# Kernel tuning notes

Measured on AMD Instinct MI355X. Metric: run time of the kernel, lower is better.

The kernel has to match this reference:

```python
import jax, jax.numpy as jnp
import numpy as np

B, S, V, F, H = 256, 512, 50000, 64, 256


def setup_inputs() -> dict:
    key = jax.random.key(0)
    ks = jax.random.split(key, 12)
    s_in = 1.0 / np.sqrt(F)
    s_hid = 1.0 / np.sqrt(H)
    return {
        "batch": jax.random.randint(ks[0], (B, S), 0, V),
        "features": jax.random.normal(ks[1], (V, F), jnp.float32),
        "W_ih0": jax.random.normal(ks[2], (H, F), jnp.float32) * s_in,
        "W_hh0": jax.random.normal(ks[3], (H, H), jnp.float32) * s_hid,
        "b_ih0": jax.random.normal(ks[4], (H,), jnp.float32) * s_hid,
        "b_hh0": jax.random.normal(ks[5], (H,), jnp.float32) * s_hid,
        "W_ih1": jax.random.normal(ks[6], (H, H), jnp.float32) * s_hid,
        "W_hh1": jax.random.normal(ks[7], (H, H), jnp.float32) * s_hid,
        "b_ih1": jax.random.normal(ks[8], (H,), jnp.float32) * s_hid,
        "b_hh1": jax.random.normal(ks[9], (H,), jnp.float32) * s_hid,
        "W_out": jax.random.normal(ks[10], (V, H), jnp.float32) * s_hid,
        "b_out": jax.random.normal(ks[11], (V,), jnp.float32) * s_hid,
    }


def _rnn_layer(x, W_ih, W_hh, b_ih, b_hh):
    # x: [B, S, Din] -> [B, S, H]; torch tanh RNN: h_t = tanh(x_t W_ih^T + b_ih + h_{t-1} W_hh^T + b_hh)
    xW = jnp.einsum('bsd,hd->bsh', x, W_ih) + (b_ih + b_hh)  # precompute input projection
    h0 = jnp.zeros((x.shape[0], W_hh.shape[0]), x.dtype)

    def step(h, xt):
        h = jnp.tanh(xt + h @ W_hh.T)
        return h, h

    _, ys = jax.lax.scan(step, h0, jnp.swapaxes(xW, 0, 1))  # scan over time
    return jnp.swapaxes(ys, 0, 1)


def reference(batch, features, W_ih0, W_hh0, b_ih0, b_hh0,
              W_ih1, W_hh1, b_ih1, b_hh1, W_out, b_out):
    # vectorized replacement of the nested per-token gather loop
    full_representation = features[batch]            # [B, S, F]
    h = _rnn_layer(full_representation, W_ih0, W_hh0, b_ih0, b_hh0)
    h = _rnn_layer(h, W_ih1, W_hh1, b_ih1, b_hh1)    # [B, S, H]
    return h[:, -1, :] @ W_out.T + b_out             # [B, V]
```

## Files before the change

kernel.cpp:

```cpp
#include <hip/hip_runtime.h>

#define B_ 256
#define S_ 512
#define V_ 50000
#define F_ 64
#define H_ 256

typedef _Float16 f16;
typedef _Float16 f16x2 __attribute__((ext_vector_type(2)));
typedef _Float16 f16x4 __attribute__((ext_vector_type(4)));
typedef _Float16 f16x8 __attribute__((ext_vector_type(8)));
typedef float f32x4 __attribute__((ext_vector_type(4)));

#define MFMA(a, b, c) __builtin_amdgcn_mfma_f32_16x16x32_f16((a), (b), (c), 0, 0, 0)

__device__ __forceinline__ f16x8 cvt8(const float4 a, const float4 b) {
    f16x8 v;
    v[0] = (f16)a.x; v[1] = (f16)a.y; v[2] = (f16)a.z; v[3] = (f16)a.w;
    v[4] = (f16)b.x; v[5] = (f16)b.y; v[6] = (f16)b.z; v[7] = (f16)b.w;
    return v;
}

__device__ __forceinline__ float fast_tanh(float x) {
    float e = __expf(2.f * x);
    float r = __builtin_amdgcn_rcpf(e + 1.f);
    return __builtin_fmaf(-2.f, r, 1.f);
}

__device__ __forceinline__ f32x4 cvt4f(const f16x4 v) {
    f32x4 r; r[0] = (float)v[0]; r[1] = (float)v[1]; r[2] = (float)v[2]; r[3] = (float)v[3];
    return r;
}
__device__ __forceinline__ f16x4 pack4s(const f32x4 a) {
    f16x4 r; r[0] = (f16)a[0]; r[1] = (f16)a[1]; r[2] = (f16)a[2]; r[3] = (f16)a[3];
    return r;
}
__device__ __forceinline__ f16x4 tanh4(const f32x4 a, const f32x4 b) {
    f16x4 r;
#pragma unroll
    for (int i = 0; i < 4; ++i) r[i] = (f16)fast_tanh(a[i] + b[i]);
    return r;
}

__global__ void k_init_flags(int* flags) {
    if (threadIdx.x < 256) flags[threadIdx.x] = 0;
}

__global__ __launch_bounds__(512) void k_vocab_proj(
    const float* __restrict__ feat, const float* __restrict__ Wih,
    const float* __restrict__ bi, const float* __restrict__ bh,
    f16* __restrict__ T)
{
    __shared__ char Wl[256 * 128];
    __shared__ char Xl[16 * 128];
    const int tid = threadIdx.x;
    {
        const int n = tid >> 1, k0 = (tid & 1) << 5;
#pragma unroll
        for (int k = k0; k < k0 + 32; k += 8) {
            float4 a = *(const float4*)(Wih + n * F_ + k);
            float4 b = *(const float4*)(Wih + n * F_ + k + 4);
            *(f16x8*)(Wl + n * 128 + (((k >> 3) ^ (n & 7)) << 4)) = cvt8(a, b);
        }
    }
    const int v0 = blockIdx.x * 16;
    {
        const int m = tid >> 5, k = (tid & 31) << 1;
        float2 a = *(const float2*)(feat + (v0 + m) * F_ + k);
        f16x2 v; v[0] = (f16)a.x; v[1] = (f16)a.y;
        *(f16x2*)(Xl + m * 128 + ((((k >> 3) ^ (m & 7)) << 4) | ((k & 7) << 1))) = v;
    }
    __syncthreads();
    const int lane = tid & 63, w = tid >> 6;
    const int q = lane & 15, g = lane >> 4;
#pragma unroll
    for (int nt = 0; nt < 2; ++nt) {
        const int n0 = w * 32 + nt * 16;
        const int nrow = n0 + q;
        float4 b1 = *(const float4*)(bi + n0 + g * 4);
        float4 b2 = *(const float4*)(bh + n0 + g * 4);
        f32x4 acc = {b1.x + b2.x, b1.y + b2.y, b1.z + b2.z, b1.w + b2.w};
#pragma unroll
        for (int kb = 0; kb < 2; ++kb) {
            f16x8 a = *(const f16x8*)(Wl + nrow * 128 + (((kb * 4 + g) ^ (nrow & 7)) << 4));
            f16x8 b = *(const f16x8*)(Xl + q * 128 + (((kb * 4 + g) ^ (q & 7)) << 4));
            acc = MFMA(a, b, acc);
        }
        f16x4 o; o[0] = (f16)acc[0]; o[1] = (f16)acc[1]; o[2] = (f16)acc[2]; o[3] = (f16)acc[3];
        *(f16x4*)(T + (size_t)(v0 + q) * H_ + n0 + g * 4) = o;
    }
}

__global__ __launch_bounds__(512) __attribute__((amdgpu_waves_per_eu(2, 2)))
void k_rnn2(
    const f16* __restrict__ T, const int* __restrict__ idx,
    const float* __restrict__ Whh0, const float* __restrict__ Wih1,
    const float* __restrict__ bih1, const float* __restrict__ bhh1,
    const float* __restrict__ Whh1,
    f16* __restrict__ h0ring, int* flags, f16* __restrict__ h1out)
{
    __shared__ char hb[2][8192];
    __shared__ char pb[2][8192];
    const int wg = blockIdx.x;
    const int tid = threadIdx.x, lane = tid & 63, w = tid >> 6;
    const int q = lane & 15, gl = lane >> 4;
    const int swz = (q & 7) << 4;

    int rbase[2];
#pragma unroll
    for (int p2 = 0; p2 < 2; ++p2)
        rbase[p2] = q * 512 + ((p2 * 64 + gl * 16) ^ swz);

    int* prodf = flags;
    int* consf = flags + 128;
    const int gr = (wg < 16) ? wg : wg - 16;
    const int brow = gr * 16 + q;
    f16* ringg = h0ring + ((size_t)gr << 19);

#define FRD(kb_, RD_) (*(const f16x8*)(hb[RD_] + rbase[(kb_) & 1] + (((kb_) >> 1) * 128)))
#define STEP_BAR() do { \
        asm volatile("s_waitcnt lgkmcnt(0)" ::: "memory"); \
        __builtin_amdgcn_s_barrier(); \
    } while (0)

    if (wg < 16) {
        const int nb2 = w * 32;
        int wb2[2];
#pragma unroll
        for (int tt = 0; tt < 2; ++tt)
            wb2[tt] = q * 512 + (((nb2 + tt * 16 + gl * 4) * 2) ^ swz);

        f16x8 wA[2][8];
#pragma unroll
        for (int tt = 0; tt < 2; ++tt) {
            const int n = nb2 + tt * 16 + q;
#pragma unroll
            for (int kb = 0; kb < 8; ++kb) {
                const int o = n * H_ + kb * 32 + gl * 8;
                wA[tt][kb] = cvt8(*(const float4*)(Whh0 + o), *(const float4*)(Whh0 + o + 4));
            }
        }
        {   f32x4 z = {0.f, 0.f, 0.f, 0.f}; *(f32x4*)(hb[1] + tid * 16) = z; }
        const int* idxr = idx + brow * S_;
        int* myflag = prodf + gr * 8 + w;
        f16x4 xa[2], xb[2];
        {
            const size_t r0 = (size_t)idxr[0] * H_, r1 = (size_t)idxr[1] * H_;
#pragma unroll
            for (int tt = 0; tt < 2; ++tt) {
                xa[tt] = *(const f16x4*)(T + r0 + nb2 + tt * 16 + gl * 4);
                xb[tt] = *(const f16x4*)(T + r1 + nb2 + tt * 16 + gl * 4);
            }
        }
        int iA = idxr[2], iB = idxr[3];
        __syncthreads();

#define PBODY(XV, ID, RD, WR, T_) do {                                          \
        if (((T_) & 15) == 0) {       \
            int v_;                                                             \
            do { v_ = __hip_atomic_load(consf + gr, __ATOMIC_RELAXED,           \
                                        __HIP_MEMORY_SCOPE_AGENT);              \
            } while ((T_) - v_ > 96);                                           \
        }                                                                       \
        f16x8 bf0 = FRD(0, RD), bf1 = FRD(1, RD), bf2 = FRD(2, RD),             \
              bf3 = FRD(3, RD), bf4 = FRD(4, RD), bf5 = FRD(5, RD),             \
              bf6 = FRD(6, RD), bf7 = FRD(7, RD);                               \
        f32x4 aL[2], aH[2];                                                     \
        _Pragma("unroll")                                                       \
        for (int tt = 0; tt < 2; ++tt) {                                        \
            aL[tt] = cvt4f(XV[tt]);                                             \
            aH[tt][0] = 0.f; aH[tt][1] = 0.f; aH[tt][2] = 0.f; aH[tt][3] = 0.f; \
        }                                                                       \
                    \
        if ((((T_) & 7) == 0) && lane == 0)                                     \
            __hip_atomic_store(myflag, (T_), __ATOMIC_RELEASE,                  \
                               __HIP_MEMORY_SCOPE_AGENT);                       \
        {                                                                       \
            const size_t rr = (size_t)ID * H_;                                  \
            _Pragma("unroll")                                                   \
            for (int tt = 0; tt < 2; ++tt)                                      \
                XV[tt] = *(const f16x4*)(T + rr + nb2 + tt * 16 + gl * 4);      \
            const int t4 = ((T_) + 4 < S_) ? (T_) + 4 : S_ - 1;                 \
            ID = idxr[t4];                                                      \
        }                                                                       \
        _Pragma("unroll")                                                       \
        for (int tt = 0; tt < 2; ++tt) {                                        \
            aL[tt] = MFMA(wA[tt][0], bf0, aL[tt]);                              \
            aH[tt] = MFMA(wA[tt][4], bf4, aH[tt]);                              \
            aL[tt] = MFMA(wA[tt][1], bf1, aL[tt]);                              \
            aH[tt] = MFMA(wA[tt][5], bf5, aH[tt]);                              \
            aL[tt] = MFMA(wA[tt][2], bf2, aL[tt]);                              \
            aH[tt] = MFMA(wA[tt][6], bf6, aH[tt]);                              \
            aL[tt] = MFMA(wA[tt][3], bf3, aL[tt]);                              \
            aH[tt] = MFMA(wA[tt][7], bf7, aH[tt]);                              \
        }                                                                       \
        {                                                                       \
            f16* rp = ringg + (size_t)((T_) & 127) * 4096 + q * 256 + nb2;      \
            _Pragma("unroll")                                                   \
            for (int tt = 0; tt < 2; ++tt) {                                    \
                f16x4 hv = tanh4(aL[tt], aH[tt]);                               \
                *(f16x4*)(hb[WR] + wb2[tt]) = hv;                               \
                *(f16x4*)(rp + tt * 16 + gl * 4) = hv;                          \
            }                                                                   \
        }                                                                       \
        STEP_BAR();                                                             \
    } while (0)

        {
            f16x8 bf0 = FRD(0, 1), bf1 = FRD(1, 1), bf2 = FRD(2, 1), bf3 = FRD(3, 1),
                  bf4 = FRD(4, 1), bf5 = FRD(5, 1), bf6 = FRD(6, 1), bf7 = FRD(7, 1);
            f32x4 aL[2], aH[2];
#pragma unroll
            for (int tt = 0; tt < 2; ++tt) {
                aL[tt] = cvt4f(xa[tt]);
                aH[tt][0] = 0.f; aH[tt][1] = 0.f; aH[tt][2] = 0.f; aH[tt][3] = 0.f;
            }
            {
                const size_t rr = (size_t)iA * H_;
#pragma unroll
                for (int tt = 0; tt < 2; ++tt)
                    xa[tt] = *(const f16x4*)(T + rr + nb2 + tt * 16 + gl * 4);
                iA = idxr[4];
            }
#pragma unroll
            for (int tt = 0; tt < 2; ++tt) {
                aL[tt] = MFMA(wA[tt][0], bf0, aL[tt]);
                aH[tt] = MFMA(wA[tt][4], bf4, aH[tt]);
                aL[tt] = MFMA(wA[tt][1], bf1, aL[tt]);
                aH[tt] = MFMA(wA[tt][5], bf5, aH[tt]);
                aL[tt] = MFMA(wA[tt][2], bf2, aL[tt]);
                aH[tt] = MFMA(wA[tt][6], bf6, aH[tt]);
                aL[tt] = MFMA(wA[tt][3], bf3, aL[tt]);
                aH[tt] = MFMA(wA[tt][7], bf7, aH[tt]);
            }
            f16* rp = ringg + q * 256 + nb2;
#pragma unroll
            for (int tt = 0; tt < 2; ++tt) {
                f16x4 hv = tanh4(aL[tt], aH[tt]);
                *(f16x4*)(hb[0] + wb2[tt]) = hv;
                *(f16x4*)(rp + tt * 16 + gl * 4) = hv;
            }
            STEP_BAR();
        }
        for (int t = 1; t < 511; t += 2) {
            PBODY(xb, iB, 0, 1, t);
            PBODY(xa, iA, 1, 0, t + 1);
        }
        PBODY(xb, iB, 0, 1, 511);
        if (lane == 0)
            __hip_atomic_store(myflag, 516, __ATOMIC_RELEASE, __HIP_MEMORY_SCOPE_AGENT);
#undef PBODY
    } else {
        const bool isC = (w < 4);
        const int nb4 = (isC ? w : w - 4) * 64;
        int xbase[4];
#pragma unroll
        for (int tt = 0; tt < 4; ++tt)
            xbase[tt] = q * 512 + (((nb4 + tt * 16 + gl * 4) * 2) ^ swz);

        f16x8 wR[4][8];
        {
            const float* Wsrc = isC ? Whh1 : Wih1;
#pragma unroll
            for (int tt = 0; tt < 4; ++tt) {
                const int n = nb4 + tt * 16 + q;
#pragma unroll
                for (int kb = 0; kb < 8; ++kb) {
                    const int o = n * H_ + kb * 32 + gl * 8;
                    wR[tt][kb] = cvt8(*(const float4*)(Wsrc + o), *(const float4*)(Wsrc + o + 4));
                }
            }
        }
        f32x4 bs1[4];
#pragma unroll
        for (int tt = 0; tt < 4; ++tt) {
            const int n = nb4 + tt * 16 + gl * 4;
            float4 x = *(const float4*)(bih1 + n);
            float4 y = *(const float4*)(bhh1 + n);
            bs1[tt][0] = x.x + y.x; bs1[tt][1] = x.y + y.y;
            bs1[tt][2] = x.z + y.z; bs1[tt][3] = x.w + y.w;
        }
        {
            f32x4 z = {0.f, 0.f, 0.f, 0.f};
            *(f32x4*)(hb[1] + tid * 16) = z;
        }

#define SPIN(need) do {                                                         \
        int mn_;                                                                \
        do {                                                                    \
            mn_ = 0x7fffffff;                                                   \
            _Pragma("unroll")                                                   \
            for (int i_ = 0; i_ < 8; ++i_) {                                    \
                int v_ = __hip_atomic_load(prodf + gr * 8 + i_, __ATOMIC_RELAXED, \
                                           __HIP_MEMORY_SCOPE_AGENT);           \
                mn_ = v_ < mn_ ? v_ : mn_;                                      \
            }                                                                   \
        } while (mn_ < (need));                                                 \
        __builtin_amdgcn_fence(__ATOMIC_ACQUIRE, "agent");                      \
    } while (0)

        f16x8 HF[8];
        if (!isC) {
            SPIN(12);
            const f16* rp = ringg + q * 256 + gl * 8;
#pragma unroll
            for (int kb = 0; kb < 8; ++kb)
                HF[kb] = *(const f16x8*)(rp + kb * 32);
        }
        __syncthreads();

#define SBODY(WRP, RDP, WRH, RDH, S_) do {                                      \
        if (isC) {                                                              \
            f16x8 cf0 = FRD(0, RDH), cf1 = FRD(1, RDH), cf2 = FRD(2, RDH),      \
                  cf3 = FRD(3, RDH), cf4 = FRD(4, RDH), cf5 = FRD(5, RDH),      \
                  cf6 = FRD(6, RDH), cf7 = FRD(7, RDH);                         \
            f32x4 cL[4], cH[4];                                                 \
            _Pragma("unroll")                                                   \
            for (int tt = 0; tt < 4; ++tt) {                                    \
                f16x4 pv = *(const f16x4*)(pb[RDP] + xbase[tt]);                \
                cL[tt] = cvt4f(pv);                                             \
                cH[tt][0] = 0.f; cH[tt][1] = 0.f; cH[tt][2] = 0.f; cH[tt][3] = 0.f; \
            }                                                                   \
            _Pragma("unroll")                                                   \
            for (int tt = 0; tt < 4; ++tt) {                                    \
                cL[tt] = MFMA(wR[tt][0], cf0, cL[tt]);                          \
                cH[tt] = MFMA(wR[tt][4], cf4, cH[tt]);                          \
                cL[tt] = MFMA(wR[tt][1], cf1, cL[tt]);                          \
                cH[tt] = MFMA(wR[tt][5], cf5, cH[tt]);                          \
                cL[tt] = MFMA(wR[tt][2], cf2, cL[tt]);                          \
                cH[tt] = MFMA(wR[tt][6], cf6, cH[tt]);                          \
                cL[tt] = MFMA(wR[tt][3], cf3, cL[tt]);                          \
                cH[tt] = MFMA(wR[tt][7], cf7, cH[tt]);                          \
            }                                                                   \
            _Pragma("unroll")                                                   \
            for (int tt = 0; tt < 4; ++tt)                                      \
                *(f16x4*)(hb[WRH] + xbase[tt]) = tanh4(cL[tt], cH[tt]);         \
            if ((tid == 0) && (((S_) & 15) == 0))                               \
                __hip_atomic_store(consf + gr, (S_), __ATOMIC_RELEASE,          \
                                   __HIP_MEMORY_SCOPE_AGENT);                   \
        } else {                                                                \
            if (((S_) & 7) == 0) {                                              \
                const int nd_ = ((S_) + 12 < 512) ? (S_) + 12 : 512;            \
                SPIN(nd_);                                                      \
            }                                                                   \
            f32x4 pA[4];                                                        \
            _Pragma("unroll")                                                   \
            for (int tt = 0; tt < 4; ++tt) pA[tt] = bs1[tt];                    \
            _Pragma("unroll")                                                   \
            for (int kb = 0; kb < 8; ++kb) {                                    \
                _Pragma("unroll")                                               \
                for (int tt = 0; tt < 4; ++tt)                                  \
                    pA[tt] = MFMA(wR[tt][kb], HF[kb], pA[tt]);                  \
            }                                                                   \
            {   \
                const int nx = ((S_) + 1 < 512) ? (S_) + 1 : 511;               \
                const f16* rp = ringg + (size_t)(nx & 127) * 4096 + q * 256 + gl * 8; \
                _Pragma("unroll")                                               \
                for (int kb = 0; kb < 8; ++kb)                                  \
                    HF[kb] = *(const f16x8*)(rp + kb * 32);                     \
            }                                                                   \
            _Pragma("unroll")                                                   \
            for (int tt = 0; tt < 4; ++tt)                                      \
                *(f16x4*)(pb[WRP] + xbase[tt]) = pack4s(pA[tt]);                \
        }                                                                       \
        STEP_BAR();                                                             \
    } while (0)

        {
            if (!isC) {
                f32x4 pA[4];
#pragma unroll
                for (int tt = 0; tt < 4; ++tt) pA[tt] = bs1[tt];
#pragma unroll
                for (int kb = 0; kb < 8; ++kb) {
#pragma unroll
                    for (int tt = 0; tt < 4; ++tt)
                        pA[tt] = MFMA(wR[tt][kb], HF[kb], pA[tt]);
                }
                {
                    const f16* rp = ringg + 4096 + q * 256 + gl * 8;
#pragma unroll
                    for (int kb = 0; kb < 8; ++kb)
                        HF[kb] = *(const f16x8*)(rp + kb * 32);
                }
#pragma unroll
                for (int tt = 0; tt < 4; ++tt)
                    *(f16x4*)(pb[0] + xbase[tt]) = pack4s(pA[tt]);
            }
            STEP_BAR();
        }
        for (int s = 1; s < 511; s += 2) {
            SBODY(1, 0, 0, 1, s);
            SBODY(0, 1, 1, 0, s + 1);
        }
        SBODY(1, 0, 0, 1, 511);
        if (isC) {
            f16x8 cf0 = FRD(0, 0), cf1 = FRD(1, 0), cf2 = FRD(2, 0), cf3 = FRD(3, 0),
                  cf4 = FRD(4, 0), cf5 = FRD(5, 0), cf6 = FRD(6, 0), cf7 = FRD(7, 0);
            f32x4 cL[4], cH[4];
#pragma unroll
            for (int tt = 0; tt < 4; ++tt) {
                f16x4 pv = *(const f16x4*)(pb[1] + xbase[tt]);
                cL[tt] = cvt4f(pv);
                cH[tt][0] = 0.f; cH[tt][1] = 0.f; cH[tt][2] = 0.f; cH[tt][3] = 0.f;
            }
#pragma unroll
            for (int tt = 0; tt < 4; ++tt) {
                cL[tt] = MFMA(wR[tt][0], cf0, cL[tt]);
                cH[tt] = MFMA(wR[tt][4], cf4, cH[tt]);
                cL[tt] = MFMA(wR[tt][1], cf1, cL[tt]);
                cH[tt] = MFMA(wR[tt][5], cf5, cH[tt]);
                cL[tt] = MFMA(wR[tt][2], cf2, cL[tt]);
                cH[tt] = MFMA(wR[tt][6], cf6, cH[tt]);
                cL[tt] = MFMA(wR[tt][3], cf3, cL[tt]);
                cH[tt] = MFMA(wR[tt][7], cf7, cH[tt]);
            }
#pragma unroll
            for (int tt = 0; tt < 4; ++tt)
                *(f16x4*)(h1out + (size_t)brow * H_ + nb4 + tt * 16 + gl * 4)
                    = tanh4(cL[tt], cH[tt]);
        }
#undef SBODY
#undef SPIN
    }
#undef FRD
#undef STEP_BAR
}

__global__ __launch_bounds__(512) void k_out(
    const f16* __restrict__ h1, const float* __restrict__ Wout,
    const float* __restrict__ bout, float* __restrict__ out)
{
    __shared__ char Hl[256 * 512];
    const int tid = threadIdx.x;
    {
        const int m = tid >> 1, half = tid & 1;
#pragma unroll
        for (int i = 0; i < 16; ++i) {
            const int blk = half * 16 + i;
            f16x8 v = *(const f16x8*)(h1 + m * H_ + blk * 8);
            *(f16x8*)(Hl + m * 512 + ((blk ^ (m & 7)) << 4)) = v;
        }
    }
    __syncthreads();
    const int lane = tid & 63, w = tid >> 6;
    const int q = lane & 15, g = lane >> 4;
    const int v0 = blockIdx.x * 80;
    f32x4 acc[5][2];
#pragma unroll
    for (int vt = 0; vt < 5; ++vt) {
        float4 bo = *(const float4*)(bout + v0 + vt * 16 + g * 4);
#pragma unroll
        for (int bt = 0; bt < 2; ++bt) {
            acc[vt][bt][0] = bo.x; acc[vt][bt][1] = bo.y;
            acc[vt][bt][2] = bo.z; acc[vt][bt][3] = bo.w;
        }
    }
#pragma unroll
    for (int kb = 0; kb < 8; ++kb) {
        f16x8 bf[2];
#pragma unroll
        for (int bt = 0; bt < 2; ++bt) {
            const int mrow = (w * 2 + bt) * 16 + q;
            bf[bt] = *(const f16x8*)(Hl + mrow * 512 + (((kb * 4 + g) ^ (mrow & 7)) << 4));
        }
#pragma unroll
        for (int vt = 0; vt < 5; ++vt) {
            const size_t vrow = v0 + vt * 16 + q;
            float4 a = *(const float4*)(Wout + vrow * H_ + kb * 32 + g * 8);
            float4 b = *(const float4*)(Wout + vrow * H_ + kb * 32 + g * 8 + 4);
            f16x8 af = cvt8(a, b);
#pragma unroll
            for (int bt = 0; bt < 2; ++bt)
                acc[vt][bt] = MFMA(af, bf[bt], acc[vt][bt]);
        }
    }
#pragma unroll
    for (int vt = 0; vt < 5; ++vt)
#pragma unroll
        for (int bt = 0; bt < 2; ++bt) {
            const int b = (w * 2 + bt) * 16 + q;
            const int v = v0 + vt * 16 + g * 4;
            float4 o = {acc[vt][bt][0], acc[vt][bt][1], acc[vt][bt][2], acc[vt][bt][3]};
            *(float4*)(out + (size_t)b * V_ + v) = o;
        }
}

extern "C" void kernel_launch(void* const* d_in, const int* in_sizes, int n_in,
                              void* d_out, int out_size, void* d_ws, size_t ws_size,
                              hipStream_t stream) {
    (void)in_sizes; (void)n_in; (void)out_size; (void)ws_size;
    const int*   batch = (const int*)  d_in[0];
    const float* feat  = (const float*)d_in[1];
    const float* Wih0  = (const float*)d_in[2];
    const float* Whh0  = (const float*)d_in[3];
    const float* bih0  = (const float*)d_in[4];
    const float* bhh0  = (const float*)d_in[5];
    const float* Wih1  = (const float*)d_in[6];
    const float* Whh1  = (const float*)d_in[7];
    const float* bih1  = (const float*)d_in[8];
    const float* bhh1  = (const float*)d_in[9];
    const float* Wout  = (const float*)d_in[10];
    const float* bout  = (const float*)d_in[11];
    float* out = (float*)d_out;

    f16* T      = (f16*)d_out;
    f16* h0ring = (f16*)((char*)d_out + 27000000);
    int* flags  = (int*)((char*)d_out + 48000000);
    f16* h1out  = (f16*)d_ws;

    k_init_flags<<<dim3(1), dim3(256), 0, stream>>>(flags);
    k_vocab_proj<<<dim3(V_ / 16), dim3(512), 0, stream>>>(feat, Wih0, bih0, bhh0, T);
    k_rnn2<<<dim3(32), dim3(512), 0, stream>>>(T, batch, Whh0, Wih1, bih1, bhh1,
                                               Whh1, h0ring, flags, h1out);
    k_out<<<dim3(625), dim3(512), 0, stream>>>(h1out, Wout, bout, out);
}
```

Before: 864.3 us.

## Split layer-1 input projection between producer and consumer workgroups

Producer (layer-0) workgroups now also compute half of the layer-1 input projection (columns 0-127) from their fresh hidden state and write it to a global buffer. Consumer workgroups compute the other half, staged through shared memory from the h0 ring. This rebalances MFMA work across the two pipeline stages and shortens the consumer critical path per step. The cost is extra global traffic and more producer work, plus a changed spin lookahead and end-flag protocol that could introduce stalls.

```diff
diff --git a/kernel.cpp b/kernel.cpp
--- a/kernel.cpp
+++ b/kernel.cpp
@@ -31,8 +31,9 @@
     f32x4 r; r[0] = (float)v[0]; r[1] = (float)v[1]; r[2] = (float)v[2]; r[3] = (float)v[3];
     return r;
 }
-__device__ __forceinline__ f16x4 pack4s(const f32x4 a) {
-    f16x4 r; r[0] = (f16)a[0]; r[1] = (f16)a[1]; r[2] = (f16)a[2]; r[3] = (f16)a[3];
+__device__ __forceinline__ f16x4 pack4(const f32x4 a, const f32x4 b) {
+    f16x4 r; r[0] = (f16)(a[0] + b[0]); r[1] = (f16)(a[1] + b[1]);
+    r[2] = (f16)(a[2] + b[2]); r[3] = (f16)(a[3] + b[3]);
     return r;
 }
 __device__ __forceinline__ f16x4 tanh4(const f32x4 a, const f32x4 b) {
@@ -97,10 +98,12 @@
     const float* __restrict__ Whh0, const float* __restrict__ Wih1,
     const float* __restrict__ bih1, const float* __restrict__ bhh1,
     const float* __restrict__ Whh1,
-    f16* __restrict__ h0ring, int* flags, f16* __restrict__ h1out)
+    f16* __restrict__ h0ring, f16* __restrict__ plow,
+    int* flags, f16* __restrict__ h1out)
 {
     __shared__ char hb[2][8192];
-    __shared__ char pb[2][8192];
+    __shared__ char h0c[2][8192];
+    __shared__ char pbb[2][4096];
     const int wg = blockIdx.x;
     const int tid = threadIdx.x, lane = tid & 63, w = tid >> 6;
     const int q = lane & 15, gl = lane >> 4;
@@ -117,7 +120,7 @@
     const int brow = gr * 16 + q;
     f16* ringg = h0ring + ((size_t)gr << 19);
 
-#define FRD(kb_, RD_) (*(const f16x8*)(hb[RD_] + rbase[(kb_) & 1] + (((kb_) >> 1) * 128)))
+#define FRDB(base_, kb_) (*(const f16x8*)((base_) + rbase[(kb_) & 1] + (((kb_) >> 1) * 128)))
 #define STEP_BAR() do { \
         asm volatile("s_waitcnt lgkmcnt(0)" ::: "memory"); \
         __builtin_amdgcn_s_barrier(); \
@@ -125,12 +128,13 @@
 
     if (wg < 16) {
         const int nb2 = w * 32;
+        const int pcol = w * 16;
         int wb2[2];
 #pragma unroll
         for (int tt = 0; tt < 2; ++tt)
             wb2[tt] = q * 512 + (((nb2 + tt * 16 + gl * 4) * 2) ^ swz);
 
-        f16x8 wA[2][8];
+        f16x8 wA[2][8], wPl[8];
 #pragma unroll
         for (int tt = 0; tt < 2; ++tt) {
             const int n = nb2 + tt * 16 + q;
@@ -139,6 +143,18 @@
                 const int o = n * H_ + kb * 32 + gl * 8;
                 wA[tt][kb] = cvt8(*(const float4*)(Whh0 + o), *(const float4*)(Whh0 + o + 4));
             }
+        }
+#pragma unroll
+        for (int kb = 0; kb < 8; ++kb) {
+            const int o = (pcol + q) * H_ + kb * 32 + gl * 8;
+            wPl[kb] = cvt8(*(const float4*)(Wih1 + o), *(const float4*)(Wih1 + o + 4));
+        }
+        f32x4 bsP;
+        {
+            const int n = pcol + gl * 4;
+            float4 x = *(const float4*)(bih1 + n);
+            float4 y = *(const float4*)(bhh1 + n);
+            bsP[0] = x.x + y.x; bsP[1] = x.y + y.y; bsP[2] = x.z + y.z; bsP[3] = x.w + y.w;
         }
         {   f32x4 z = {0.f, 0.f, 0.f, 0.f}; *(f32x4*)(hb[1] + tid * 16) = z; }
         const int* idxr = idx + brow * S_;
@@ -162,16 +178,15 @@
                                         __HIP_MEMORY_SCOPE_AGENT);              \
             } while ((T_) - v_ > 96);                                           \
         }                                                                       \
-        f16x8 bf0 = FRD(0, RD), bf1 = FRD(1, RD), bf2 = FRD(2, RD),             \
-              bf3 = FRD(3, RD), bf4 = FRD(4, RD), bf5 = FRD(5, RD),             \
-              bf6 = FRD(6, RD), bf7 = FRD(7, RD);                               \
+        f16x8 bf0 = FRDB(hb[RD], 0), bf1 = FRDB(hb[RD], 1), bf2 = FRDB(hb[RD], 2), \
+              bf3 = FRDB(hb[RD], 3), bf4 = FRDB(hb[RD], 4), bf5 = FRDB(hb[RD], 5), \
+              bf6 = FRDB(hb[RD], 6), bf7 = FRDB(hb[RD], 7);                     \
         f32x4 aL[2], aH[2];                                                     \
         _Pragma("unroll")                                                       \
         for (int tt = 0; tt < 2; ++tt) {                                        \
             aL[tt] = cvt4f(XV[tt]);                                             \
             aH[tt][0] = 0.f; aH[tt][1] = 0.f; aH[tt][2] = 0.f; aH[tt][3] = 0.f; \
         }                                                                       \
-                    \
         if ((((T_) & 7) == 0) && lane == 0)                                     \
             __hip_atomic_store(myflag, (T_), __ATOMIC_RELEASE,                  \
                                __HIP_MEMORY_SCOPE_AGENT);                       \
@@ -194,6 +209,13 @@
             aL[tt] = MFMA(wA[tt][3], bf3, aL[tt]);                              \
             aH[tt] = MFMA(wA[tt][7], bf7, aH[tt]);                              \
         }                                                                       \
+                    \
+        f32x4 pLx = bsP, pHx;                                                   \
+        pHx[0] = 0.f; pHx[1] = 0.f; pHx[2] = 0.f; pHx[3] = 0.f;                 \
+        pLx = MFMA(wPl[0], bf0, pLx);  pHx = MFMA(wPl[4], bf4, pHx);            \
+        pLx = MFMA(wPl[1], bf1, pLx);  pHx = MFMA(wPl[5], bf5, pHx);            \
+        pLx = MFMA(wPl[2], bf2, pLx);  pHx = MFMA(wPl[6], bf6, pHx);            \
+        pLx = MFMA(wPl[3], bf3, pLx);  pHx = MFMA(wPl[7], bf7, pHx);            \
         {                                                                       \
             f16* rp = ringg + (size_t)((T_) & 127) * 4096 + q * 256 + nb2;      \
             _Pragma("unroll")                                                   \
@@ -202,13 +224,16 @@
                 *(f16x4*)(hb[WR] + wb2[tt]) = hv;                               \
                 *(f16x4*)(rp + tt * 16 + gl * 4) = hv;                          \
             }                                                                   \
+            *(f16x4*)(plow + ((size_t)brow * 512 + (T_) - 1) * 128              \
+                      + pcol + gl * 4) = pack4(pLx, pHx);                       \
         }                                                                       \
         STEP_BAR();                                                             \
     } while (0)
 
         {
-            f16x8 bf0 = FRD(0, 1), bf1 = FRD(1, 1), bf2 = FRD(2, 1), bf3 = FRD(3, 1),
-                  bf4 = FRD(4, 1), bf5 = FRD(5, 1), bf6 = FRD(6, 1), bf7 = FRD(7, 1);
+            f16x8 bf0 = FRDB(hb[1], 0), bf1 = FRDB(hb[1], 1), bf2 = FRDB(hb[1], 2),
+                  bf3 = FRDB(hb[1], 3), bf4 = FRDB(hb[1], 4), bf5 = FRDB(hb[1], 5),
+                  bf6 = FRDB(hb[1], 6), bf7 = FRDB(hb[1], 7);
             f32x4 aL[2], aH[2];
 #pragma unroll
             for (int tt = 0; tt < 2; ++tt) {
@@ -247,43 +272,62 @@
             PBODY(xa, iA, 1, 0, t + 1);
         }
         PBODY(xb, iB, 0, 1, 511);
+        {
+            f16x8 bf0 = FRDB(hb[1], 0), bf1 = FRDB(hb[1], 1), bf2 = FRDB(hb[1], 2),
+                  bf3 = FRDB(hb[1], 3), bf4 = FRDB(hb[1], 4), bf5 = FRDB(hb[1], 5),
+                  bf6 = FRDB(hb[1], 6), bf7 = FRDB(hb[1], 7);
+            f32x4 pLx = bsP, pHx;
+            pHx[0] = 0.f; pHx[1] = 0.f; pHx[2] = 0.f; pHx[3] = 0.f;
+            pLx = MFMA(wPl[0], bf0, pLx);  pHx = MFMA(wPl[4], bf4, pHx);
+            pLx = MFMA(wPl[1], bf1, pLx);  pHx = MFMA(wPl[5], bf5, pHx);
+            pLx = MFMA(wPl[2], bf2, pLx);  pHx = MFMA(wPl[6], bf6, pHx);
+            pLx = MFMA(wPl[3], bf3, pLx);  pHx = MFMA(wPl[7], bf7, pHx);
+            *(f16x4*)(plow + ((size_t)brow * 512 + 511) * 128 + pcol + gl * 4)
+                = pack4(pLx, pHx);
+        }
         if (lane == 0)
-            __hip_atomic_store(myflag, 516, __ATOMIC_RELEASE, __HIP_MEMORY_SCOPE_AGENT);
+            __hip_atomic_store(myflag, 512, __ATOMIC_RELEASE, __HIP_MEMORY_SCOPE_AGENT);
 #undef PBODY
     } else {
         const bool isC = (w < 4);
-        const int nb4 = (isC ? w : w - 4) * 64;
+        const int stg_r = tid >> 5, stg_c = tid & 31;
+        const int stg_addr = stg_r * 512 + ((stg_c ^ (stg_r & 7)) << 4);
+        const int pj = w - 4;
+        const int nb4 = w * 64;
         int xbase[4];
 #pragma unroll
         for (int tt = 0; tt < 4; ++tt)
-            xbase[tt] = q * 512 + (((nb4 + tt * 16 + gl * 4) * 2) ^ swz);
+            xbase[tt] = q * 512 + ((((isC ? nb4 : 0) + tt * 16 + gl * 4) * 2) ^ swz);
 
         f16x8 wR[4][8];
-        {
-            const float* Wsrc = isC ? Whh1 : Wih1;
+        f32x4 bsPh[2];
+        if (isC) {
 #pragma unroll
             for (int tt = 0; tt < 4; ++tt) {
                 const int n = nb4 + tt * 16 + q;
 #pragma unroll
                 for (int kb = 0; kb < 8; ++kb) {
                     const int o = n * H_ + kb * 32 + gl * 8;
-                    wR[tt][kb] = cvt8(*(const float4*)(Wsrc + o), *(const float4*)(Wsrc + o + 4));
+                    wR[tt][kb] = cvt8(*(const float4*)(Whh1 + o), *(const float4*)(Whh1 + o + 4));
                 }
             }
-        }
-        f32x4 bs1[4];
-#pragma unroll
-        for (int tt = 0; tt < 4; ++tt) {
-            const int n = nb4 + tt * 16 + gl * 4;
-            float4 x = *(const float4*)(bih1 + n);
-            float4 y = *(const float4*)(bhh1 + n);
-            bs1[tt][0] = x.x + y.x; bs1[tt][1] = x.y + y.y;
-            bs1[tt][2] = x.z + y.z; bs1[tt][3] = x.w + y.w;
-        }
-        {
-            f32x4 z = {0.f, 0.f, 0.f, 0.f};
-            *(f32x4*)(hb[1] + tid * 16) = z;
-        }
+        } else {
+#pragma unroll
+            for (int tt = 0; tt < 2; ++tt) {
+                const int n = 128 + pj * 32 + tt * 16 + q;
+#pragma unroll
+                for (int kb = 0; kb < 8; ++kb) {
+                    const int o = n * H_ + kb * 32 + gl * 8;
+                    wR[tt][kb] = cvt8(*(const float4*)(Wih1 + o), *(const float4*)(Wih1 + o + 4));
+                }
+                const int nb = 128 + pj * 32 + tt * 16 + gl * 4;
+                float4 x = *(const float4*)(bih1 + nb);
+                float4 y = *(const float4*)(bhh1 + nb);
+                bsPh[tt][0] = x.x + y.x; bsPh[tt][1] = x.y + y.y;
+                bsPh[tt][2] = x.z + y.z; bsPh[tt][3] = x.w + y.w;
+            }
+        }
+        {   f32x4 z = {0.f, 0.f, 0.f, 0.f}; *(f32x4*)(hb[1] + tid * 16) = z; }
 
 #define SPIN(need) do {                                                         \
         int mn_;                                                                \
@@ -299,28 +343,51 @@
         __builtin_amdgcn_fence(__ATOMIC_ACQUIRE, "agent");                      \
     } while (0)
 
-        f16x8 HF[8];
-        if (!isC) {
-            SPIN(12);
-            const f16* rp = ringg + q * 256 + gl * 8;
-#pragma unroll
-            for (int kb = 0; kb < 8; ++kb)
-                HF[kb] = *(const f16x8*)(rp + kb * 32);
+        f16x4 pvE[4], pvO[4];
+        SPIN(13);
+        {
+            f16x8 sreg = *(const f16x8*)(ringg + (size_t)tid * 8);
+            if (isC && w < 2) {
+#pragma unroll
+                for (int tt = 0; tt < 4; ++tt) {
+                    pvE[tt] = *(const f16x4*)(plow + ((size_t)brow * 512 + 0) * 128
+                                              + nb4 + tt * 16 + gl * 4);
+                    pvO[tt] = *(const f16x4*)(plow + ((size_t)brow * 512 + 1) * 128
+                                              + nb4 + tt * 16 + gl * 4);
+                }
+            }
+            *(f16x8*)(h0c[0] + stg_addr) = sreg;
         }
         __syncthreads();
 
-#define SBODY(WRP, RDP, WRH, RDH, S_) do {                                      \
+#define CSTEP(PV, PAR, S_) do {                                                 \
+        if (((S_) & 7) == 1) {                                                  \
+            const int nd_ = ((S_) + 11 < 512) ? (S_) + 11 : 512;                \
+            SPIN(nd_);                                                          \
+        }                                                                       \
+        const int sl_ = ((S_) + 1 < 512) ? (S_) + 1 : 511;                      \
+        f16x8 sreg = *(const f16x8*)(ringg + (size_t)(sl_ & 127) * 4096 + (size_t)tid * 8); \
         if (isC) {                                                              \
-            f16x8 cf0 = FRD(0, RDH), cf1 = FRD(1, RDH), cf2 = FRD(2, RDH),      \
-                  cf3 = FRD(3, RDH), cf4 = FRD(4, RDH), cf5 = FRD(5, RDH),      \
-                  cf6 = FRD(6, RDH), cf7 = FRD(7, RDH);                         \
             f32x4 cL[4], cH[4];                                                 \
+            if (w < 2) {                                                        \
+                _Pragma("unroll")                                               \
+                for (int tt = 0; tt < 4; ++tt) cL[tt] = cvt4f(PV[tt]);          \
+            } else {                                                            \
+                _Pragma("unroll")                                               \
+                for (int tt = 0; tt < 4; ++tt) {                                \
+                    f16x4 pv_ = *(const f16x4*)(pbb[1 - (PAR)]                  \
+                        + ((16 * (w - 2) + 4 * tt + gl) * 16 + q) * 8);         \
+                    cL[tt] = cvt4f(pv_);                                        \
+                }                                                               \
+            }                                                                   \
             _Pragma("unroll")                                                   \
             for (int tt = 0; tt < 4; ++tt) {                                    \
-                f16x4 pv = *(const f16x4*)(pb[RDP] + xbase[tt]);                \
-                cL[tt] = cvt4f(pv);                                             \
                 cH[tt][0] = 0.f; cH[tt][1] = 0.f; cH[tt][2] = 0.f; cH[tt][3] = 0.f; \
             }                                                                   \
+            f16x8 cf0 = FRDB(hb[PAR], 0), cf1 = FRDB(hb[PAR], 1),               \
+                  cf2 = FRDB(hb[PAR], 2), cf3 = FRDB(hb[PAR], 3),               \
+                  cf4 = FRDB(hb[PAR], 4), cf5 = FRDB(hb[PAR], 5),               \
+                  cf6 = FRDB(hb[PAR], 6), cf7 = FRDB(hb[PAR], 7);               \
             _Pragma("unroll")                                                   \
             for (int tt = 0; tt < 4; ++tt) {                                    \
                 cL[tt] = MFMA(wR[tt][0], cf0, cL[tt]);                          \
@@ -332,78 +399,98 @@
                 cL[tt] = MFMA(wR[tt][3], cf3, cL[tt]);                          \
                 cH[tt] = MFMA(wR[tt][7], cf7, cH[tt]);                          \
             }                                                                   \
+            if (w < 2) {            \
+                const int tr = ((S_) + 1 < 512) ? (S_) + 1 : 511;               \
+                _Pragma("unroll")                                               \
+                for (int tt = 0; tt < 4; ++tt)                                  \
+                    PV[tt] = *(const f16x4*)(plow + ((size_t)brow * 512 + tr) * 128 \
+                                             + nb4 + tt * 16 + gl * 4);         \
+            }                                                                   \
             _Pragma("unroll")                                                   \
             for (int tt = 0; tt < 4; ++tt)                                      \
-                *(f16x4*)(hb[WRH] + xbase[tt]) = tanh4(cL[tt], cH[tt]);         \
+                *(f16x4*)(hb[1 - (PAR)] + xbase[tt]) = tanh4(cL[tt], cH[tt]);   \
             if ((tid == 0) && (((S_) & 15) == 0))                               \
                 __hip_atomic_store(consf + gr, (S_), __ATOMIC_RELEASE,          \
                                    __HIP_MEMORY_SCOPE_AGENT);                   \
         } else {                                                                \
-            if (((S_) & 7) == 0) {                                              \
-                const int nd_ = ((S_) + 12 < 512) ? (S_) + 12 : 512;            \
-                SPIN(nd_);                                                      \
+            f16x8 hf0 = FRDB(h0c[PAR], 0), hf1 = FRDB(h0c[PAR], 1),             \
+                  hf2 = FRDB(h0c[PAR], 2), hf3 = FRDB(h0c[PAR], 3),             \
+                  hf4 = FRDB(h0c[PAR], 4), hf5 = FRDB(h0c[PAR], 5),             \
+                  hf6 = FRDB(h0c[PAR], 6), hf7 = FRDB(h0c[PAR], 7);             \
+            f32x4 pL[2], pH[2];                                                 \
+            _Pragma("unroll")                                                   \
+            for (int tt = 0; tt < 2; ++tt) {                                    \
+                pL[tt] = bsPh[tt];                                              \
+                pH[tt][0] = 0.f; pH[tt][1] = 0.f; pH[tt][2] = 0.f; pH[tt][3] = 0.f; \
+                pL[tt] = MFMA(wR[tt][0], hf0, pL[tt]);                          \
+                pH[tt] = MFMA(wR[tt][4], hf4, pH[tt]);                          \
+                pL[tt] = MFMA(wR[tt][1], hf1, pL[tt]);                          \
+                pH[tt] = MFMA(wR[tt][5], hf5, pH[tt]);                          \
+                pL[tt] = MFMA(wR[tt][2], hf2, pL[tt]);                          \
+                pH[tt] = MFMA(wR[tt][6], hf6, pH[tt]);                          \
+                pL[tt] = MFMA(wR[tt][3], hf3, pL[tt]);                          \
+                pH[tt] = MFMA(wR[tt][7], hf7, pH[tt]);                          \
+                *(f16x4*)(pbb[PAR] + ((8 * pj + 4 * tt + gl) * 16 + q) * 8)     \
+                    = pack4(pL[tt], pH[tt]);                                    \
             }                                                                   \
-            f32x4 pA[4];                                                        \
-            _Pragma("unroll")                                                   \
-            for (int tt = 0; tt < 4; ++tt) pA[tt] = bs1[tt];                    \
-            _Pragma("unroll")                                                   \
-            for (int kb = 0; kb < 8; ++kb) {                                    \
-                _Pragma("unroll")                                               \
-                for (int tt = 0; tt < 4; ++tt)                                  \
-                    pA[tt] = MFMA(wR[tt][kb], HF[kb], pA[tt]);                  \
-            }                                                                   \
-            {   \
-                const int nx = ((S_) + 1 < 512) ? (S_) + 1 : 511;               \
-                const f16* rp = ringg + (size_t)(nx & 127) * 4096 + q * 256 + gl * 8; \
-                _Pragma("unroll")                                               \
-                for (int kb = 0; kb < 8; ++kb)                                  \
-                    HF[kb] = *(const f16x8*)(rp + kb * 32);                     \
-            }                                                                   \
-            _Pragma("unroll")                                                   \
-            for (int tt = 0; tt < 4; ++tt)                                      \
-                *(f16x4*)(pb[WRP] + xbase[tt]) = pack4s(pA[tt]);                \
         }                                                                       \
+        *(f16x8*)(h0c[1 - (PAR)] + stg_addr) = sreg;                            \
         STEP_BAR();                                                             \
     } while (0)
 
         {
+            f16x8 sreg = *(const f16x8*)(ringg + (size_t)4096 + (size_t)tid * 8);
             if (!isC) {
-                f32x4 pA[4];
-#pragma unroll
-                for (int tt = 0; tt < 4; ++tt) pA[tt] = bs1[tt];
-#pragma unroll
-                for (int kb = 0; kb < 8; ++kb) {
-#pragma unroll
-                    for (int tt = 0; tt < 4; ++tt)
-                        pA[tt] = MFMA(wR[tt][kb], HF[kb], pA[tt]);
+                f16x8 hf0 = FRDB(h0c[0], 0), hf1 = FRDB(h0c[0], 1),
+                      hf2 = FRDB(h0c[0], 2), hf3 = FRDB(h0c[0], 3),
+                      hf4 = FRDB(h0c[0], 4), hf5 = FRDB(h0c[0], 5),
+                      hf6 = FRDB(h0c[0], 6), hf7 = FRDB(h0c[0], 7);
+                f32x4 pL[2], pH[2];
+#pragma unroll
+                for (int tt = 0; tt < 2; ++tt) {
+                    pL[tt] = bsPh[tt];
+                    pH[tt][0] = 0.f; pH[tt][1] = 0.f; pH[tt][2] = 0.f; pH[tt][3] = 0.f;
+                    pL[tt] = MFMA(wR[tt][0], hf0, pL[tt]);
+                    pH[tt] = MFMA(wR[tt][4], hf4, pH[tt]);
+                    pL[tt] = MFMA(wR[tt][1], hf1, pL[tt]);
+                    pH[tt] = MFMA(wR[tt][5], hf5, pH[tt]);
+                    pL[tt] = MFMA(wR[tt][2], hf2, pL[tt]);
+                    pH[tt] = MFMA(wR[tt][6], hf6, pH[tt]);
+                    pL[tt] = MFMA(wR[tt][3], hf3, pL[tt]);
+                    pH[tt] = MFMA(wR[tt][7], hf7, pH[tt]);
+                    *(f16x4*)(pbb[0] + ((8 * pj + 4 * tt + gl) * 16 + q) * 8)
+                        = pack4(pL[tt], pH[tt]);
                 }
-                {
-                    const f16* rp = ringg + 4096 + q * 256 + gl * 8;
-#pragma unroll
-                    for (int kb = 0; kb < 8; ++kb)
-                        HF[kb] = *(const f16x8*)(rp + kb * 32);
+            }
+            *(f16x8*)(h0c[1] + stg_addr) = sreg;
+            STEP_BAR();
+        }
+        for (int s = 1; s < 511; s += 2) {
+            CSTEP(pvE, 1, s);
+            CSTEP(pvO, 0, s + 1);
+        }
+        CSTEP(pvE, 1, 511);
+        if (isC) {
+            f32x4 cL[4], cH[4];
+            if (w < 2) {
+#pragma unroll
+                for (int tt = 0; tt < 4; ++tt) cL[tt] = cvt4f(pvO[tt]);
+            } else {
+#pragma unroll
+                for (int tt = 0; tt < 4; ++tt) {
+                    f16x4 pv_ = *(const f16x4*)(pbb[1]
+                        + ((16 * (w - 2) + 4 * tt + gl) * 16 + q) * 8);
+                    cL[tt] = cvt4f(pv_);
                 }
-#pragma unroll
-                for (int tt = 0; tt < 4; ++tt)
-                    *(f16x4*)(pb[0] + xbase[tt]) = pack4s(pA[tt]);
-            }
-            STEP_BAR();
-        }
-        for (int s = 1; s < 511; s += 2) {
-            SBODY(1, 0, 0, 1, s);
-            SBODY(0, 1, 1, 0, s + 1);
-        }
-        SBODY(1, 0, 0, 1, 511);
-        if (isC) {
-            f16x8 cf0 = FRD(0, 0), cf1 = FRD(1, 0), cf2 = FRD(2, 0), cf3 = FRD(3, 0),
-                  cf4 = FRD(4, 0), cf5 = FRD(5, 0), cf6 = FRD(6, 0), cf7 = FRD(7, 0);
-            f32x4 cL[4], cH[4];
+            }
 #pragma unroll
             for (int tt = 0; tt < 4; ++tt) {
-                f16x4 pv = *(const f16x4*)(pb[1] + xbase[tt]);
-                cL[tt] = cvt4f(pv);
                 cH[tt][0] = 0.f; cH[tt][1] = 0.f; cH[tt][2] = 0.f; cH[tt][3] = 0.f;
             }
+            f16x8 cf0 = FRDB(hb[0], 0), cf1 = FRDB(hb[0], 1),
+                  cf2 = FRDB(hb[0], 2), cf3 = FRDB(hb[0], 3),
+                  cf4 = FRDB(hb[0], 4), cf5 = FRDB(hb[0], 5),
+                  cf6 = FRDB(hb[0], 6), cf7 = FRDB(hb[0], 7);
 #pragma unroll
             for (int tt = 0; tt < 4; ++tt) {
                 cL[tt] = MFMA(wR[tt][0], cf0, cL[tt]);
@@ -420,10 +507,12 @@
                 *(f16x4*)(h1out + (size_t)brow * H_ + nb4 + tt * 16 + gl * 4)
                     = tanh4(cL[tt], cH[tt]);
         }
-#undef SBODY
+        if (isC && tid == 0)
+            __hip_atomic_store(consf + gr, 512, __ATOMIC_RELEASE, __HIP_MEMORY_SCOPE_AGENT);
+#undef CSTEP
 #undef SPIN
     }
-#undef FRD
+#undef FRDB
 #undef STEP_BAR
 }
 
@@ -507,11 +596,12 @@
     f16* T      = (f16*)d_out;
     f16* h0ring = (f16*)((char*)d_out + 27000000);
     int* flags  = (int*)((char*)d_out + 48000000);
-    f16* h1out  = (f16*)d_ws;
+    f16* plow   = (f16*)d_ws;
+    f16* h1out  = (f16*)((char*)d_ws + (size_t)B_ * S_ * 128 * 2);
 
     k_init_flags<<<dim3(1), dim3(256), 0, stream>>>(flags);
     k_vocab_proj<<<dim3(V_ / 16), dim3(512), 0, stream>>>(feat, Wih0, bih0, bhh0, T);
     k_rnn2<<<dim3(32), dim3(512), 0, stream>>>(T, batch, Whh0, Wih1, bih1, bhh1,
-                                               Whh1, h0ring, flags, h1out);
+                                               Whh1, h0ring, plow, flags, h1out);
     k_out<<<dim3(625), dim3(512), 0, stream>>>(h1out, Wout, bout, out);
 }
```

New measurement: 1.028 ms. +18.9%, slower.
